# Performance work log

Hardware: AMD Instinct MI355X
Metric: run time of the kernel (lower is better)

## Reference

```python
import jax, jax.numpy as jnp
import numpy as np

T, B, D_IN, D_LAT = 512, 64, 512, 1024


def setup_inputs() -> dict:
    key = jax.random.key(0)
    ks = jax.random.split(key, 5)
    scale = 1.0 / np.sqrt(D_IN + D_LAT)
    inp = {"x": jax.random.normal(ks[0], (T, B, D_IN), dtype=jnp.float32)}
    for name, k in zip(("Wf", "Wi", "Wo", "Wu"), ks[1:]):
        inp[name] = jax.random.normal(k, (D_IN + D_LAT, D_LAT), dtype=jnp.float32) * scale
    for name in ("bf", "bi", "bo", "bu"):
        inp[name] = jnp.zeros((D_LAT,), dtype=jnp.float32)
    return inp


def reference(x, Wf, bf, Wi, bi, Wo, bo, Wu, bu):
    # x: [T, B, D_in]; returns history of hidden states [T, B, D_lat]
    lat = Wf.shape[1]
    h0 = jnp.zeros((x.shape[1], lat), dtype=x.dtype)
    c0 = jnp.zeros((x.shape[1], lat), dtype=x.dtype)

    def step(carry, xt):
        h, c = carry
        z = jnp.concatenate([xt, h], axis=-1)            # [B, D_in + D_lat]
        ft = jax.nn.sigmoid(z @ Wf + bf)                 # forget gate
        it = jax.nn.sigmoid(z @ Wi + bi)                 # input gate
        ut = jnp.tanh(z @ Wu + bu)                       # candidate update
        ct = ft * c + it * ut
        ot = jax.nn.sigmoid(z @ Wo + bo)                 # output gate
        ht = ot * jnp.tanh(ct)
        return (ht, ct), ht

    _, hist = jax.lax.scan(step, (h0, c0), x)
    return hist
```

## Files before the change

kernel.cpp:

```cpp
#include <hip/hip_runtime.h>
#include <hip/hip_bf16.h>
#include <stdint.h>

#define T_STEPS 512
#define BATCH   64
#define DIN     512
#define DLAT    1024
#define NWG     256
#define NSLOT   64

typedef __bf16 bf16_t;
typedef __bf16 bf16x4 __attribute__((ext_vector_type(4)));
typedef __bf16 bf16x8 __attribute__((ext_vector_type(8)));
typedef float  f32x4  __attribute__((ext_vector_type(4)));
typedef uint32_t u32x4 __attribute__((ext_vector_type(4)));

#define XB_OFF     0u
#define WXT_OFF    33554432u
#define HWT_OFF    (WXT_OFF + 4194304u)
#define HS_OFF     (HWT_OFF + 8388608u)
#define SLOT_ELEMS 65536
#define MEMSET_BYTES 8388608u

#define PART_OFF_B 0
#define LDS_BYTES  131072

__global__ void xconv_kernel(const float* __restrict__ x, bf16_t* __restrict__ xb) {
    size_t i = ((size_t)blockIdx.x * 256 + threadIdx.x) * 4;
    const float4 v = *(const float4*)(x + i);
    bf16x4 o;
    o[0] = (bf16_t)v.x; o[1] = (bf16_t)v.y; o[2] = (bf16_t)v.z; o[3] = (bf16_t)v.w;
    *(bf16x4*)(xb + i) = o;
}

__global__ void wxt_prep(const float* __restrict__ Wf, const float* __restrict__ Wi,
                         const float* __restrict__ Wo, const float* __restrict__ Wu,
                         bf16_t* __restrict__ wxt) {
    const int gid  = blockIdx.x * 256 + threadIdx.x;
    const int lane = gid & 63;
    const int f    = gid >> 6;
    const int cf   = f & 3;
    const int ks   = (f >> 2) & 3;
    const int wv   = (f >> 4) & 3;
    const int ct   = f >> 6;
    const float* Wg = (cf == 0) ? Wf : (cf == 1) ? Wi : (cf == 2) ? Wo : Wu;
    const int k0 = wv * 128 + ks * 32 + (lane >> 4) * 8;
    const int j  = ct * 16 + (lane & 15);
    bf16x8 v;
#pragma unroll
    for (int e = 0; e < 8; ++e) v[e] = (bf16_t)Wg[(size_t)(k0 + e) * DLAT + j];
    *(bf16x8*)(wxt + (size_t)gid * 8) = v;
}

__global__ void hwt_prep(const float* __restrict__ Wf, const float* __restrict__ Wi,
                         const float* __restrict__ Wo, const float* __restrict__ Wu,
                         bf16_t* __restrict__ hwt) {
    const int gid  = blockIdx.x * 256 + threadIdx.x;
    const int lane = gid & 63;
    const int f    = gid >> 6;
    const int cf   = f & 3;
    const int ks   = (f >> 2) & 7;
    const int wv   = (f >> 5) & 3;
    const int ct   = f >> 7;
    const float* Wg = (cf == 0) ? Wf : (cf == 1) ? Wi : (cf == 2) ? Wo : Wu;
    const int k0 = 512 + wv * 256 + ks * 32 + (lane >> 4) * 8;
    const int j  = ct * 16 + (lane & 15);
    bf16x8 v;
#pragma unroll
    for (int e = 0; e < 8; ++e) v[e] = (bf16_t)Wg[(size_t)(k0 + e) * DLAT + j];
    *(bf16x8*)(hwt + (size_t)gid * 8) = v;
}

__device__ __forceinline__ float rcp_(float x) { return __builtin_amdgcn_rcpf(x); }
__device__ __forceinline__ float sigmoidf_(float v) { return rcp_(1.f + __expf(-v)); }
__device__ __forceinline__ float tanh_fast(float x) {
    const float ax = fabsf(x);
    const float e  = __expf(-2.f * ax);
    const float t  = (1.f - e) * rcp_(1.f + e);
    return copysignf(t, x);
}

__device__ __forceinline__ bf16x8 ldh16_sc1(const bf16_t* p) {
    f32x4 r;
    asm volatile("global_load_dwordx4 %0, %1, off sc1"
                 : "=v"(r) : "v"(p) : "memory");
    return __builtin_bit_cast(bf16x8, r);
}

__device__ __forceinline__ void sth2u(bf16_t* p, uint32_t bits) {
    asm volatile("global_store_short %0, %1, off sc1"
                 :: "v"(p), "v"(bits) : "memory");
}

__device__ __forceinline__ void bar_lds() {
    asm volatile("s_waitcnt lgkmcnt(0)" ::: "memory");
    __builtin_amdgcn_s_barrier();
    asm volatile("" ::: "memory");
}

__launch_bounds__(256, 1)
__global__ void lstm_main(const float* __restrict__ bfp, const float* __restrict__ bip,
                          const float* __restrict__ bop, const float* __restrict__ bup,
                          const bf16_t* __restrict__ xb,
                          const bf16_t* __restrict__ wxt,
                          const bf16_t* __restrict__ hwt,
                          bf16_t* __restrict__ hslots,
                          float* __restrict__ out) {
    extern __shared__ char ldsraw[];
    float* part = (float*)(ldsraw + PART_OFF_B);

    const int tid  = threadIdx.x;
    const int wv   = tid >> 6;
    const int lane = tid & 63;
    const int lm   = lane & 15;
    const int lq   = lane >> 4;
    const int rb   = blockIdx.x & 3;
    const int ct   = blockIdx.x >> 2;
    const int r0   = rb * 16;
    const int j0   = ct * 16;

    const int row_l = tid >> 4;
    const int jj    = tid & 15;
    const float bias_r[4] = { bfp[j0 + jj], bip[j0 + jj], bop[j0 + jj], bup[j0 + jj] };
    float cst = 0.f;

    bf16x8 hwr[32];
    {
        const bf16_t* hw_base = hwt + (size_t)((ct * 4 + wv) * 32) * 512;
#pragma unroll
        for (int f = 0; f < 32; ++f)
            hwr[f] = *(const bf16x8*)(hw_base + (size_t)f * 512 + lane * 8);
    }
    bf16x8 wxr[16];
    {
        const bf16_t* wx_base = wxt + (size_t)((ct * 4 + wv) * 16) * 512;
#pragma unroll
        for (int f = 0; f < 16; ++f)
            wxr[f] = *(const bf16x8*)(wx_base + (size_t)f * 512 + lane * 8);
    }

    f32x4 acc[4];
#pragma unroll
    for (int cf = 0; cf < 4; ++cf) acc[cf] = (f32x4){0.f, 0.f, 0.f, 0.f};

    {
        const bf16_t* xa = xb + (size_t)(r0 + lm) * DIN + wv * 128 + lq * 8;
#pragma unroll
        for (int ks = 0; ks < 4; ++ks) {
            const bf16x8 a = *(const bf16x8*)(xa + ks * 32);
#pragma unroll
            for (int cf = 0; cf < 4; ++cf)
                acc[cf] = __builtin_amdgcn_mfma_f32_16x16x32_bf16(a, wxr[ks * 4 + cf], acc[cf], 0, 0, 0);
        }
    }

    for (int t = 0; t < T_STEPS; ++t) {
        const bf16_t* hprev = hslots + (size_t)(t & (NSLOT - 1)) * SLOT_ELEMS;
        bf16_t*       hnext = hslots + (size_t)((t + 1) & (NSLOT - 1)) * SLOT_ELEMS;
        bf16_t*       zslot = hslots + (size_t)((t + 2) & (NSLOT - 1)) * SLOT_ELEMS;

        if (t > 0) {
            const bf16_t* hb = hprev + (size_t)(r0 + lm) * DLAT + wv * 256 + lq * 8;
            bf16x8 ha[8];
            while (true) {
#pragma unroll
                for (int ks = 0; ks < 8; ++ks) ha[ks] = ldh16_sc1(hb + ks * 32);
                asm volatile("s_waitcnt vmcnt(0)" ::: "memory");
                __builtin_amdgcn_sched_barrier(0);
                bool ok = true;
#pragma unroll
                for (int ks = 0; ks < 8; ++ks) {
                    const u32x4 w = __builtin_bit_cast(u32x4, ha[ks]);
#pragma unroll
                    for (int i = 0; i < 4; ++i)
                        ok = ok && ((w[i] & 0xFFFFu) != 0u) && ((w[i] & 0xFFFF0000u) != 0u);
                }
                if (__all(ok)) break;
            }
#pragma unroll
            for (int ks = 0; ks < 8; ++ks)
#pragma unroll
                for (int cf = 0; cf < 4; ++cf)
                    acc[cf] = __builtin_amdgcn_mfma_f32_16x16x32_bf16(ha[ks], hwr[ks * 4 + cf], acc[cf], 0, 0, 0);
        }

#pragma unroll
        for (int cf = 0; cf < 4; ++cf)
            *(f32x4*)&part[(wv * 64 + cf * 16 + lm) * 20 + lq * 4] = acc[cf];
        bar_lds();

        float gs[4];
#pragma unroll
        for (int g = 0; g < 4; ++g) {
            const int c = g * 16 + jj;
            gs[g] = part[(0 * 64 + c) * 20 + row_l] + part[(1 * 64 + c) * 20 + row_l]
                  + part[(2 * 64 + c) * 20 + row_l] + part[(3 * 64 + c) * 20 + row_l]
                  + bias_r[g];
        }
        const float ft = sigmoidf_(gs[0]);
        const float it = sigmoidf_(gs[1]);
        const float ot = sigmoidf_(gs[2]);
        const float ut = tanh_fast(gs[3]);
        cst = ft * cst + it * ut;
        const float hv = ot * tanh_fast(cst);

        {
            uint32_t hbits = (uint32_t)__builtin_bit_cast(uint16_t, (bf16_t)hv);
            if (hbits == 0u) hbits = 0x8000u;
            sth2u(hnext + (size_t)(r0 + row_l) * DLAT + j0 + jj, hbits);
        }
        sth2u(zslot + (size_t)(r0 + row_l) * DLAT + j0 + jj, 0u);

        bar_lds();

        out[((size_t)t * BATCH + r0 + row_l) * DLAT + j0 + jj] = hv;

#pragma unroll
        for (int cf = 0; cf < 4; ++cf) acc[cf] = (f32x4){0.f, 0.f, 0.f, 0.f};
        if (t + 1 < T_STEPS) {
            const bf16_t* xa = xb + (size_t)(t + 1) * (BATCH * DIN)
                             + (size_t)(r0 + lm) * DIN + wv * 128 + lq * 8;
#pragma unroll
            for (int ks = 0; ks < 4; ++ks) {
                const bf16x8 a = *(const bf16x8*)(xa + ks * 32);
#pragma unroll
                for (int cf = 0; cf < 4; ++cf)
                    acc[cf] = __builtin_amdgcn_mfma_f32_16x16x32_bf16(a, wxr[ks * 4 + cf], acc[cf], 0, 0, 0);
            }
        }
    }
}

extern "C" void kernel_launch(void* const* d_in, const int* in_sizes, int n_in,
                              void* d_out, int out_size, void* d_ws, size_t ws_size,
                              hipStream_t stream) {
    const float* x  = (const float*)d_in[0];
    const float* Wf = (const float*)d_in[1];
    const float* Wi = (const float*)d_in[2];
    const float* Wo = (const float*)d_in[3];
    const float* Wu = (const float*)d_in[4];
    const float* bf = (const float*)d_in[5];
    const float* bi = (const float*)d_in[6];
    const float* bo = (const float*)d_in[7];
    const float* bu = (const float*)d_in[8];
    float* out = (float*)d_out;

    char* ws = (char*)d_ws;
    bf16_t* xb     = (bf16_t*)(ws + XB_OFF);
    bf16_t* wxt    = (bf16_t*)(ws + WXT_OFF);
    bf16_t* hwt    = (bf16_t*)(ws + HWT_OFF);
    bf16_t* hslots = (bf16_t*)(ws + HS_OFF);

    (void)hipMemsetAsync(ws + HS_OFF, 0, MEMSET_BYTES, stream);

    xconv_kernel<<<16384, 256, 0, stream>>>(x, xb);
    wxt_prep<<<1024, 256, 0, stream>>>(Wf, Wi, Wo, Wu, wxt);
    hwt_prep<<<2048, 256, 0, stream>>>(Wf, Wi, Wo, Wu, hwt);

    (void)hipFuncSetAttribute((const void*)lstm_main,
                              hipFuncAttributeMaxDynamicSharedMemorySize, LDS_BYTES);

    lstm_main<<<NWG, 256, LDS_BYTES, stream>>>(bf, bi, bo, bu,
                                               xb, wxt, hwt, hslots, out);
}
```

Measured before the change: 1.553 ms.

## Overlap next-step x projection with h polling via double-buffered accumulators

Restructures the time loop so each step issues the next step's x-input loads together with the h-state polling loads, and computes the x·Wx MFMAs for step t+1 into a second accumulator while the h loads are still in flight. The LDS partial buffer is double-buffered by step parity, which removes the second barrier per step. Global stores now go through inline asm. The aim is to shorten the serial critical path per recurrent step, at the cost of more registers and subtler memory-ordering assumptions.

```diff
diff --git a/kernel.cpp b/kernel.cpp
--- a/kernel.cpp
+++ b/kernel.cpp
@@ -22,7 +22,7 @@
 #define SLOT_ELEMS 65536
 #define MEMSET_BYTES 8388608u
 
-#define PART_OFF_B 0
+#define PART_STRIDE_F 5120
 #define LDS_BYTES  131072
 
 __global__ void xconv_kernel(const float* __restrict__ x, bf16_t* __restrict__ xb) {
@@ -80,22 +80,40 @@
     return copysignf(t, x);
 }
 
-__device__ __forceinline__ bf16x8 ldh16_sc1(const bf16_t* p) {
+__device__ __forceinline__ void ld16_sc1(const bf16_t* p, bf16x8& d) {
     f32x4 r;
-    asm volatile("global_load_dwordx4 %0, %1, off sc1"
-                 : "=v"(r) : "v"(p) : "memory");
-    return __builtin_bit_cast(bf16x8, r);
-}
-
-__device__ __forceinline__ void sth2u(bf16_t* p, uint32_t bits) {
-    asm volatile("global_store_short %0, %1, off sc1"
-                 :: "v"(p), "v"(bits) : "memory");
-}
+    asm volatile("global_load_dwordx4 %0, %1, off sc1" : "=v"(r) : "v"(p) : "memory");
+    d = __builtin_bit_cast(bf16x8, r);
+}
+__device__ __forceinline__ void ld16_c(const bf16_t* p, bf16x8& d) {
+    f32x4 r;
+    asm volatile("global_load_dwordx4 %0, %1, off" : "=v"(r) : "v"(p) : "memory");
+    d = __builtin_bit_cast(bf16x8, r);
+}
+__device__ __forceinline__ void st2_sc1(bf16_t* p, uint32_t bits) {
+    asm volatile("global_store_short %0, %1, off sc1" :: "v"(p), "v"(bits) : "memory");
+}
+__device__ __forceinline__ void st4_c(float* p, float v) {
+    asm volatile("global_store_dword %0, %1, off" :: "v"(p), "v"(v) : "memory");
+}
+#define VMCNT(n) asm volatile("s_waitcnt vmcnt(" #n ")" ::: "memory")
 
 __device__ __forceinline__ void bar_lds() {
     asm volatile("s_waitcnt lgkmcnt(0)" ::: "memory");
     __builtin_amdgcn_s_barrier();
     asm volatile("" ::: "memory");
+}
+
+__device__ __forceinline__ bool check_h(const bf16x8 (&ha)[8]) {
+    bool ok = true;
+#pragma unroll
+    for (int ks = 0; ks < 8; ++ks) {
+        const u32x4 w = __builtin_bit_cast(u32x4, ha[ks]);
+#pragma unroll
+        for (int i = 0; i < 4; ++i)
+            ok = ok && ((w[i] & 0xFFFFu) != 0u) && ((w[i] & 0xFFFF0000u) != 0u);
+    }
+    return ok;
 }
 
 __launch_bounds__(256, 1)
@@ -107,7 +125,7 @@
                           bf16_t* __restrict__ hslots,
                           float* __restrict__ out) {
     extern __shared__ char ldsraw[];
-    float* part = (float*)(ldsraw + PART_OFF_B);
+    float* part = (float*)ldsraw;
 
     const int tid  = threadIdx.x;
     const int wv   = tid >> 6;
@@ -139,62 +157,27 @@
             wxr[f] = *(const bf16x8*)(wx_base + (size_t)f * 512 + lane * 8);
     }
 
-    f32x4 acc[4];
-#pragma unroll
-    for (int cf = 0; cf < 4; ++cf) acc[cf] = (f32x4){0.f, 0.f, 0.f, 0.f};
-
-    {
-        const bf16_t* xa = xb + (size_t)(r0 + lm) * DIN + wv * 128 + lq * 8;
-#pragma unroll
-        for (int ks = 0; ks < 4; ++ks) {
-            const bf16x8 a = *(const bf16x8*)(xa + ks * 32);
-#pragma unroll
-            for (int cf = 0; cf < 4; ++cf)
-                acc[cf] = __builtin_amdgcn_mfma_f32_16x16x32_bf16(a, wxr[ks * 4 + cf], acc[cf], 0, 0, 0);
-        }
-    }
-
-    for (int t = 0; t < T_STEPS; ++t) {
-        const bf16_t* hprev = hslots + (size_t)(t & (NSLOT - 1)) * SLOT_ELEMS;
-        bf16_t*       hnext = hslots + (size_t)((t + 1) & (NSLOT - 1)) * SLOT_ELEMS;
-        bf16_t*       zslot = hslots + (size_t)((t + 2) & (NSLOT - 1)) * SLOT_ELEMS;
-
-        if (t > 0) {
-            const bf16_t* hb = hprev + (size_t)(r0 + lm) * DLAT + wv * 256 + lq * 8;
-            bf16x8 ha[8];
-            while (true) {
-#pragma unroll
-                for (int ks = 0; ks < 8; ++ks) ha[ks] = ldh16_sc1(hb + ks * 32);
-                asm volatile("s_waitcnt vmcnt(0)" ::: "memory");
-                __builtin_amdgcn_sched_barrier(0);
-                bool ok = true;
-#pragma unroll
-                for (int ks = 0; ks < 8; ++ks) {
-                    const u32x4 w = __builtin_bit_cast(u32x4, ha[ks]);
-#pragma unroll
-                    for (int i = 0; i < 4; ++i)
-                        ok = ok && ((w[i] & 0xFFFFu) != 0u) && ((w[i] & 0xFFFF0000u) != 0u);
-                }
-                if (__all(ok)) break;
-            }
-#pragma unroll
-            for (int ks = 0; ks < 8; ++ks)
-#pragma unroll
-                for (int cf = 0; cf < 4; ++cf)
-                    acc[cf] = __builtin_amdgcn_mfma_f32_16x16x32_bf16(ha[ks], hwr[ks * 4 + cf], acc[cf], 0, 0, 0);
-        }
-
+    f32x4 acc0[4], acc1[4];
+#pragma unroll
+    for (int cf = 0; cf < 4; ++cf) {
+        acc0[cf] = (f32x4){0.f, 0.f, 0.f, 0.f};
+        acc1[cf] = (f32x4){0.f, 0.f, 0.f, 0.f};
+    }
+
+    auto finish = [&](int t, f32x4 (&acc)[4]) {
+        bf16_t* hnext = hslots + (size_t)((t + 1) & (NSLOT - 1)) * SLOT_ELEMS;
+        bf16_t* zslot = hslots + (size_t)((t + 2) & (NSLOT - 1)) * SLOT_ELEMS;
+        float* pb = part + (size_t)(t & 1) * PART_STRIDE_F;
 #pragma unroll
         for (int cf = 0; cf < 4; ++cf)
-            *(f32x4*)&part[(wv * 64 + cf * 16 + lm) * 20 + lq * 4] = acc[cf];
+            *(f32x4*)&pb[(wv * 64 + cf * 16 + lm) * 20 + lq * 4] = acc[cf];
         bar_lds();
-
         float gs[4];
 #pragma unroll
         for (int g = 0; g < 4; ++g) {
             const int c = g * 16 + jj;
-            gs[g] = part[(0 * 64 + c) * 20 + row_l] + part[(1 * 64 + c) * 20 + row_l]
-                  + part[(2 * 64 + c) * 20 + row_l] + part[(3 * 64 + c) * 20 + row_l]
+            gs[g] = pb[(0 * 64 + c) * 20 + row_l] + pb[(1 * 64 + c) * 20 + row_l]
+                  + pb[(2 * 64 + c) * 20 + row_l] + pb[(3 * 64 + c) * 20 + row_l]
                   + bias_r[g];
         }
         const float ft = sigmoidf_(gs[0]);
@@ -203,32 +186,83 @@
         const float ut = tanh_fast(gs[3]);
         cst = ft * cst + it * ut;
         const float hv = ot * tanh_fast(cst);
-
-        {
-            uint32_t hbits = (uint32_t)__builtin_bit_cast(uint16_t, (bf16_t)hv);
-            if (hbits == 0u) hbits = 0x8000u;
-            sth2u(hnext + (size_t)(r0 + row_l) * DLAT + j0 + jj, hbits);
-        }
-        sth2u(zslot + (size_t)(r0 + row_l) * DLAT + j0 + jj, 0u);
-
-        bar_lds();
-
-        out[((size_t)t * BATCH + r0 + row_l) * DLAT + j0 + jj] = hv;
-
+        uint32_t hbits = (uint32_t)__builtin_bit_cast(uint16_t, (bf16_t)hv);
+        if (hbits == 0u) hbits = 0x8000u;
+        st2_sc1(hnext + (size_t)(r0 + row_l) * DLAT + j0 + jj, hbits);
+        st2_sc1(zslot + (size_t)(r0 + row_l) * DLAT + j0 + jj, 0u);
+        st4_c(out + ((size_t)t * BATCH + r0 + row_l) * DLAT + j0 + jj, hv);
 #pragma unroll
         for (int cf = 0; cf < 4; ++cf) acc[cf] = (f32x4){0.f, 0.f, 0.f, 0.f};
-        if (t + 1 < T_STEPS) {
-            const bf16_t* xa = xb + (size_t)(t + 1) * (BATCH * DIN)
-                             + (size_t)(r0 + lm) * DIN + wv * 128 + lq * 8;
-#pragma unroll
-            for (int ks = 0; ks < 4; ++ks) {
-                const bf16x8 a = *(const bf16x8*)(xa + ks * 32);
-#pragma unroll
-                for (int cf = 0; cf < 4; ++cf)
-                    acc[cf] = __builtin_amdgcn_mfma_f32_16x16x32_bf16(a, wxr[ks * 4 + cf], acc[cf], 0, 0, 0);
-            }
-        }
-    }
+    };
+
+    auto body = [&](int t, f32x4 (&acc)[4], f32x4 (&accN)[4]) {
+        const bf16_t* hprev = hslots + (size_t)(t & (NSLOT - 1)) * SLOT_ELEMS;
+        const int tn = (t + 1 < T_STEPS) ? (t + 1) : (T_STEPS - 1);
+
+        bf16x8 xa[4];
+        const bf16_t* xsrc = xb + (size_t)tn * (BATCH * DIN)
+                           + (size_t)(r0 + lm) * DIN + wv * 128 + lq * 8;
+#pragma unroll
+        for (int ks = 0; ks < 4; ++ks) ld16_c(xsrc + ks * 32, xa[ks]);
+        bf16x8 ha[8];
+        const bf16_t* hb = hprev + (size_t)(r0 + lm) * DLAT + wv * 256 + lq * 8;
+#pragma unroll
+        for (int ks = 0; ks < 8; ++ks) ld16_sc1(hb + ks * 32, ha[ks]);
+
+        VMCNT(8);
+        __builtin_amdgcn_sched_barrier(0);
+#pragma unroll
+        for (int ks = 0; ks < 4; ++ks)
+#pragma unroll
+            for (int cf = 0; cf < 4; ++cf)
+                accN[cf] = __builtin_amdgcn_mfma_f32_16x16x32_bf16(xa[ks], wxr[ks * 4 + cf], accN[cf], 0, 0, 0);
+
+        VMCNT(0);
+        __builtin_amdgcn_sched_barrier(0);
+        while (!__all(check_h(ha))) {
+#pragma unroll
+            for (int ks = 0; ks < 8; ++ks) ld16_sc1(hb + ks * 32, ha[ks]);
+            VMCNT(0);
+            __builtin_amdgcn_sched_barrier(0);
+        }
+#pragma unroll
+        for (int ks = 0; ks < 8; ++ks)
+#pragma unroll
+            for (int cf = 0; cf < 4; ++cf)
+                acc[cf] = __builtin_amdgcn_mfma_f32_16x16x32_bf16(ha[ks], hwr[ks * 4 + cf], acc[cf], 0, 0, 0);
+
+        finish(t, acc);
+    };
+
+    {
+        const bf16_t* xa = xb + (size_t)(r0 + lm) * DIN + wv * 128 + lq * 8;
+#pragma unroll
+        for (int ks = 0; ks < 4; ++ks) {
+            const bf16x8 a = *(const bf16x8*)(xa + ks * 32);
+#pragma unroll
+            for (int cf = 0; cf < 4; ++cf)
+                acc0[cf] = __builtin_amdgcn_mfma_f32_16x16x32_bf16(a, wxr[ks * 4 + cf], acc0[cf], 0, 0, 0);
+        }
+    }
+    finish(0, acc0);
+    VMCNT(0);
+    {
+        const bf16_t* xa = xb + (size_t)(BATCH * DIN)
+                         + (size_t)(r0 + lm) * DIN + wv * 128 + lq * 8;
+#pragma unroll
+        for (int ks = 0; ks < 4; ++ks) {
+            const bf16x8 a = *(const bf16x8*)(xa + ks * 32);
+#pragma unroll
+            for (int cf = 0; cf < 4; ++cf)
+                acc0[cf] = __builtin_amdgcn_mfma_f32_16x16x32_bf16(a, wxr[ks * 4 + cf], acc0[cf], 0, 0, 0);
+        }
+    }
+
+    for (int t = 1; t < T_STEPS - 1; t += 2) {
+        body(t,     acc0, acc1);
+        body(t + 1, acc1, acc0);
+    }
+    body(T_STEPS - 1, acc0, acc1);
 }
 
 extern "C" void kernel_launch(void* const* d_in, const int* in_sizes, int n_in,
```

Result: slower. 2.322 ms (+49.5%).

## Double-buffer LDS partials, drop second barrier, prefetch next x during recurrence

Applied to the files above, without the earlier changes.

Restructures the recurrent loop so the LDS partial-sum buffer alternates between two halves by timestep parity, which removes the second per-step barrier. The next step's x tile is loaded right after the h spin-wait and before the h MFMAs, hiding its latency behind the recurrent matmul and the gate math. The x-projection MFMAs for step t+1 are issued after the h store. The risk is extra registers for the prefetched x and weaker ordering between the LDS read and the next write, which relies on the parity buffers.

```diff
diff --git a/kernel.cpp b/kernel.cpp
--- a/kernel.cpp
+++ b/kernel.cpp
@@ -22,7 +22,7 @@
 #define SLOT_ELEMS 65536
 #define MEMSET_BYTES 8388608u
 
-#define PART_OFF_B 0
+#define PART_STRIDE_F 5120
 #define LDS_BYTES  131072
 
 __global__ void xconv_kernel(const float* __restrict__ x, bf16_t* __restrict__ xb) {
@@ -107,7 +107,7 @@
                           bf16_t* __restrict__ hslots,
                           float* __restrict__ out) {
     extern __shared__ char ldsraw[];
-    float* part = (float*)(ldsraw + PART_OFF_B);
+    float* part = (float*)ldsraw;
 
     const int tid  = threadIdx.x;
     const int wv   = tid >> 6;
@@ -143,58 +143,20 @@
 #pragma unroll
     for (int cf = 0; cf < 4; ++cf) acc[cf] = (f32x4){0.f, 0.f, 0.f, 0.f};
 
-    {
-        const bf16_t* xa = xb + (size_t)(r0 + lm) * DIN + wv * 128 + lq * 8;
-#pragma unroll
-        for (int ks = 0; ks < 4; ++ks) {
-            const bf16x8 a = *(const bf16x8*)(xa + ks * 32);
-#pragma unroll
-            for (int cf = 0; cf < 4; ++cf)
-                acc[cf] = __builtin_amdgcn_mfma_f32_16x16x32_bf16(a, wxr[ks * 4 + cf], acc[cf], 0, 0, 0);
-        }
-    }
-
-    for (int t = 0; t < T_STEPS; ++t) {
-        const bf16_t* hprev = hslots + (size_t)(t & (NSLOT - 1)) * SLOT_ELEMS;
-        bf16_t*       hnext = hslots + (size_t)((t + 1) & (NSLOT - 1)) * SLOT_ELEMS;
-        bf16_t*       zslot = hslots + (size_t)((t + 2) & (NSLOT - 1)) * SLOT_ELEMS;
-
-        if (t > 0) {
-            const bf16_t* hb = hprev + (size_t)(r0 + lm) * DLAT + wv * 256 + lq * 8;
-            bf16x8 ha[8];
-            while (true) {
-#pragma unroll
-                for (int ks = 0; ks < 8; ++ks) ha[ks] = ldh16_sc1(hb + ks * 32);
-                asm volatile("s_waitcnt vmcnt(0)" ::: "memory");
-                __builtin_amdgcn_sched_barrier(0);
-                bool ok = true;
-#pragma unroll
-                for (int ks = 0; ks < 8; ++ks) {
-                    const u32x4 w = __builtin_bit_cast(u32x4, ha[ks]);
-#pragma unroll
-                    for (int i = 0; i < 4; ++i)
-                        ok = ok && ((w[i] & 0xFFFFu) != 0u) && ((w[i] & 0xFFFF0000u) != 0u);
-                }
-                if (__all(ok)) break;
-            }
-#pragma unroll
-            for (int ks = 0; ks < 8; ++ks)
-#pragma unroll
-                for (int cf = 0; cf < 4; ++cf)
-                    acc[cf] = __builtin_amdgcn_mfma_f32_16x16x32_bf16(ha[ks], hwr[ks * 4 + cf], acc[cf], 0, 0, 0);
-        }
-
+    auto finish = [&](int t, f32x4 (&a)[4]) {
+        bf16_t* hnext = hslots + (size_t)((t + 1) & (NSLOT - 1)) * SLOT_ELEMS;
+        bf16_t* zslot = hslots + (size_t)((t + 2) & (NSLOT - 1)) * SLOT_ELEMS;
+        float* pb = part + (size_t)(t & 1) * PART_STRIDE_F;
 #pragma unroll
         for (int cf = 0; cf < 4; ++cf)
-            *(f32x4*)&part[(wv * 64 + cf * 16 + lm) * 20 + lq * 4] = acc[cf];
+            *(f32x4*)&pb[(wv * 64 + cf * 16 + lm) * 20 + lq * 4] = a[cf];
         bar_lds();
-
         float gs[4];
 #pragma unroll
         for (int g = 0; g < 4; ++g) {
             const int c = g * 16 + jj;
-            gs[g] = part[(0 * 64 + c) * 20 + row_l] + part[(1 * 64 + c) * 20 + row_l]
-                  + part[(2 * 64 + c) * 20 + row_l] + part[(3 * 64 + c) * 20 + row_l]
+            gs[g] = pb[(0 * 64 + c) * 20 + row_l] + pb[(1 * 64 + c) * 20 + row_l]
+                  + pb[(2 * 64 + c) * 20 + row_l] + pb[(3 * 64 + c) * 20 + row_l]
                   + bias_r[g];
         }
         const float ft = sigmoidf_(gs[0]);
@@ -203,31 +165,82 @@
         const float ut = tanh_fast(gs[3]);
         cst = ft * cst + it * ut;
         const float hv = ot * tanh_fast(cst);
-
+        uint32_t hbits = (uint32_t)__builtin_bit_cast(uint16_t, (bf16_t)hv);
+        if (hbits == 0u) hbits = 0x8000u;
+        sth2u(hnext + (size_t)(r0 + row_l) * DLAT + j0 + jj, hbits);
+        sth2u(zslot + (size_t)(r0 + row_l) * DLAT + j0 + jj, 0u);
+        out[((size_t)t * BATCH + r0 + row_l) * DLAT + j0 + jj] = hv;
+#pragma unroll
+        for (int cf = 0; cf < 4; ++cf) a[cf] = (f32x4){0.f, 0.f, 0.f, 0.f};
+    };
+
+    {
+        const bf16_t* xa = xb + (size_t)(r0 + lm) * DIN + wv * 128 + lq * 8;
+#pragma unroll
+        for (int ks = 0; ks < 4; ++ks) {
+            const bf16x8 a = *(const bf16x8*)(xa + ks * 32);
+#pragma unroll
+            for (int cf = 0; cf < 4; ++cf)
+                acc[cf] = __builtin_amdgcn_mfma_f32_16x16x32_bf16(a, wxr[ks * 4 + cf], acc[cf], 0, 0, 0);
+        }
+    }
+    finish(0, acc);
+    asm volatile("s_waitcnt vmcnt(0)" ::: "memory");
+    {
+        const bf16_t* xa = xb + (size_t)(BATCH * DIN)
+                         + (size_t)(r0 + lm) * DIN + wv * 128 + lq * 8;
+#pragma unroll
+        for (int ks = 0; ks < 4; ++ks) {
+            const bf16x8 a = *(const bf16x8*)(xa + ks * 32);
+#pragma unroll
+            for (int cf = 0; cf < 4; ++cf)
+                acc[cf] = __builtin_amdgcn_mfma_f32_16x16x32_bf16(a, wxr[ks * 4 + cf], acc[cf], 0, 0, 0);
+        }
+    }
+
+    for (int t = 1; t < T_STEPS; ++t) {
+        const bf16_t* hprev = hslots + (size_t)(t & (NSLOT - 1)) * SLOT_ELEMS;
+        const int tn = (t + 1 < T_STEPS) ? (t + 1) : (T_STEPS - 1);
+
+        const bf16_t* hb = hprev + (size_t)(r0 + lm) * DLAT + wv * 256 + lq * 8;
+        bf16x8 ha[8];
+        while (true) {
+#pragma unroll
+            for (int ks = 0; ks < 8; ++ks) ha[ks] = ldh16_sc1(hb + ks * 32);
+            asm volatile("s_waitcnt vmcnt(0)" ::: "memory");
+            __builtin_amdgcn_sched_barrier(0);
+            bool ok = true;
+#pragma unroll
+            for (int ks = 0; ks < 8; ++ks) {
+                const u32x4 w = __builtin_bit_cast(u32x4, ha[ks]);
+#pragma unroll
+                for (int i = 0; i < 4; ++i)
+                    ok = ok && ((w[i] & 0xFFFFu) != 0u) && ((w[i] & 0xFFFF0000u) != 0u);
+            }
+            if (__all(ok)) break;
+        }
+
+        bf16x8 xv[4];
         {
-            uint32_t hbits = (uint32_t)__builtin_bit_cast(uint16_t, (bf16_t)hv);
-            if (hbits == 0u) hbits = 0x8000u;
-            sth2u(hnext + (size_t)(r0 + row_l) * DLAT + j0 + jj, hbits);
-        }
-        sth2u(zslot + (size_t)(r0 + row_l) * DLAT + j0 + jj, 0u);
-
-        bar_lds();
-
-        out[((size_t)t * BATCH + r0 + row_l) * DLAT + j0 + jj] = hv;
-
-#pragma unroll
-        for (int cf = 0; cf < 4; ++cf) acc[cf] = (f32x4){0.f, 0.f, 0.f, 0.f};
-        if (t + 1 < T_STEPS) {
-            const bf16_t* xa = xb + (size_t)(t + 1) * (BATCH * DIN)
-                             + (size_t)(r0 + lm) * DIN + wv * 128 + lq * 8;
-#pragma unroll
-            for (int ks = 0; ks < 4; ++ks) {
-                const bf16x8 a = *(const bf16x8*)(xa + ks * 32);
-#pragma unroll
-                for (int cf = 0; cf < 4; ++cf)
-                    acc[cf] = __builtin_amdgcn_mfma_f32_16x16x32_bf16(a, wxr[ks * 4 + cf], acc[cf], 0, 0, 0);
-            }
-        }
+            const bf16_t* xsrc = xb + (size_t)tn * (BATCH * DIN)
+                               + (size_t)(r0 + lm) * DIN + wv * 128 + lq * 8;
+#pragma unroll
+            for (int ks = 0; ks < 4; ++ks) xv[ks] = *(const bf16x8*)(xsrc + ks * 32);
+        }
+
+#pragma unroll
+        for (int ks = 0; ks < 8; ++ks)
+#pragma unroll
+            for (int cf = 0; cf < 4; ++cf)
+                acc[cf] = __builtin_amdgcn_mfma_f32_16x16x32_bf16(ha[ks], hwr[ks * 4 + cf], acc[cf], 0, 0, 0);
+
+        finish(t, acc);
+
+#pragma unroll
+        for (int ks = 0; ks < 4; ++ks)
+#pragma unroll
+            for (int cf = 0; cf < 4; ++cf)
+                acc[cf] = __builtin_amdgcn_mfma_f32_16x16x32_bf16(xv[ks], wxr[ks * 4 + cf], acc[cf], 0, 0, 0);
     }
 }
 
```

New measurement: 1.642 ms. 5.8% more time.
